# Kernel tuning notes

Hardware: AMD Instinct MI355X
Metric: run time of the kernel (lower is better)

## Reference

```python
import jax, jax.numpy as jnp
import numpy as np

B, N = 4, 512
C_IN, RES, SR = 256, 7, 2
FC_DIM = 1024
NUM_CLASSES, BOX_DIM, BINS = 3, 6, 12
OUT_CH = NUM_CLASSES * (1 + BOX_DIM + 2 * BINS) + 1  # 94
IMG = 512
STRIDES = (8, 16, 32)


def setup_inputs() -> dict:
    key = jax.random.key(0)
    ks = jax.random.split(key, 12)
    feat_p3 = jax.random.normal(ks[0], (B, C_IN, IMG // 8, IMG // 8), jnp.float32)
    feat_p4 = jax.random.normal(ks[1], (B, C_IN, IMG // 16, IMG // 16), jnp.float32)
    feat_p5 = jax.random.normal(ks[2], (B, C_IN, IMG // 32, IMG // 32), jnp.float32)
    cy = jax.random.uniform(ks[3], (B, N), minval=64.0, maxval=448.0)
    cx = jax.random.uniform(ks[4], (B, N), minval=64.0, maxval=448.0)
    h = jax.random.uniform(ks[5], (B, N), minval=16.0, maxval=120.0)
    w = jax.random.uniform(ks[6], (B, N), minval=16.0, maxval=120.0)
    bbox2d = jnp.stack([cy - h / 2, cx - w / 2, cy + h / 2, cx + w / 2], -1)  # tlbr
    anchors = jnp.stack([cy, cx, h, w], -1)  # (y, x, l, w)
    anchor_id = jax.random.randint(ks[7], (B, N), 0, 9, dtype=jnp.int32)
    flat = C_IN * RES * RES
    fc1_w = jax.random.normal(ks[8], (FC_DIM, flat), jnp.float32) * 0.01
    fc1_b = jnp.zeros((FC_DIM,), jnp.float32)
    bn1_g = jnp.ones((FC_DIM,), jnp.float32)
    bn1_b = jnp.zeros((FC_DIM,), jnp.float32)
    fc2_w = jax.random.normal(ks[9], (FC_DIM, FC_DIM), jnp.float32) * 0.02
    fc2_b = jnp.zeros((FC_DIM,), jnp.float32)
    bn2_g = jnp.ones((FC_DIM,), jnp.float32)
    bn2_b = jnp.zeros((FC_DIM,), jnp.float32)
    pred_w = jax.random.normal(ks[10], (OUT_CH, FC_DIM), jnp.float32) * 0.02
    pred_b = jnp.zeros((OUT_CH,), jnp.float32)
    return dict(feat_p3=feat_p3, feat_p4=feat_p4, feat_p5=feat_p5, bbox2d=bbox2d,
                anchors=anchors, anchor_id=anchor_id, fc1_w=fc1_w, fc1_b=fc1_b,
                bn1_g=bn1_g, bn1_b=bn1_b, fc2_w=fc2_w, fc2_b=fc2_b,
                bn2_g=bn2_g, bn2_b=bn2_b, pred_w=pred_w, pred_b=pred_b)


def _roi_align(feat, boxes, scale):
    # feat: [C,H,W]; boxes: [N,4] tlbr in image coords; aligned=True ROIAlign.
    C, H, W = feat.shape
    S = RES * SR
    t = boxes[:, 0] * scale - 0.5
    l = boxes[:, 1] * scale - 0.5
    bh = (boxes[:, 2] - boxes[:, 0]) * scale / RES  # bin height
    bw = (boxes[:, 3] - boxes[:, 1]) * scale / RES
    g = (jnp.arange(S, dtype=feat.dtype) + 0.5) / SR  # sample offsets in bin units
    ys = t[:, None] + g[None, :] * bh[:, None]  # [N,S]
    xs = l[:, None] + g[None, :] * bw[:, None]
    yc = jnp.clip(ys, 0.0, H - 1.0)
    xc = jnp.clip(xs, 0.0, W - 1.0)
    y0 = jnp.floor(yc)
    x0 = jnp.floor(xc)
    y0i = y0.astype(jnp.int32)
    x0i = x0.astype(jnp.int32)
    y1i = jnp.minimum(y0i + 1, H - 1)
    x1i = jnp.minimum(x0i + 1, W - 1)
    ly = yc - y0
    lx = xc - x0

    def gat(yi, xi):  # -> [C,N,S,S]
        return feat[:, yi[:, :, None], xi[:, None, :]]

    w00 = ((1 - ly)[:, :, None] * (1 - lx)[:, None, :])[None]
    w01 = ((1 - ly)[:, :, None] * lx[:, None, :])[None]
    w10 = (ly[:, :, None] * (1 - lx)[:, None, :])[None]
    w11 = (ly[:, :, None] * lx[:, None, :])[None]
    v = gat(y0i, x0i) * w00 + gat(y0i, x1i) * w01 + gat(y1i, x0i) * w10 + gat(y1i, x1i) * w11
    v = jnp.transpose(v, (1, 0, 2, 3)).reshape(-1, C, RES, SR, RES, SR)
    return v.mean((3, 5))  # [N,C,RES,RES] avg over sampling grid


def _bn_train(x, g, b):
    m = x.mean(0)
    v = x.var(0)
    return (x - m) * jax.lax.rsqrt(v + 1e-5) * g + b


def _forward(feat_p3, feat_p4, feat_p5, bbox2d, anchors, fc1_w, fc1_b, bn1_g, bn1_b,
             fc2_w, fc2_b, bn2_g, bn2_b, pred_w, pred_b, anchor_id):
    feats = (feat_p3, feat_p4, feat_p5)
    lvl = anchor_id // 3  # [B,N] feature-level assignment
    # box_pooler: pool every box at every level, then select its assigned level
    # (equivalent to the torch gather/sort/cat dispatch, in original box order).
    sel = 0.0
    for i, s in enumerate(STRIDES):
        pooled = jax.vmap(lambda f, bx, sc=1.0 / s: _roi_align(f, bx, sc))(feats[i], bbox2d)
        sel = sel + pooled * (lvl == i)[..., None, None, None].astype(pooled.dtype)
    x = sel.reshape(B * N, -1)  # [B*N, C*7*7]
    x = jax.nn.relu(_bn_train(x @ fc1_w.T + fc1_b, bn1_g, bn1_b))
    x = jax.nn.relu(_bn_train(x @ fc2_w.T + fc2_b, bn2_g, bn2_b))
    pred = (x @ pred_w.T + pred_b).reshape(B, N, OUT_CH)
    # decode: slice per-loss channels then apply box deltas per category
    c0 = NUM_CLASSES + 1
    cat = pred[..., :c0]  # [B,N,4]
    b1 = c0 + NUM_CLASSES * BOX_DIM
    bbox3d = pred[..., c0:b1].reshape(B, N, NUM_CLASSES, BOX_DIM)
    yaw_cls = pred[..., b1:b1 + NUM_CLASSES * BINS]
    yaw_res = pred[..., b1 + NUM_CLASSES * BINS:]
    delta = bbox3d[..., :4]  # yxlw deltas per category
    zh = bbox3d[..., 4:]
    stride_px = jnp.exp2(lvl.astype(pred.dtype) + 3.0)  # 8/16/32
    yx = anchors[:, :, None, :2] + delta[..., :2] * stride_px[..., None, None]
    lw = anchors[:, :, None, 2:] * jnp.exp(jnp.clip(delta[..., 2:], -4.0, 4.0))
    box_out = jnp.concatenate([yx, lw, zh], -1).reshape(B, N, NUM_CLASSES * BOX_DIM)
    return jnp.concatenate([cat, box_out, yaw_cls, yaw_res], -1)  # [B,N,94]


def reference(feat_p3, feat_p4, feat_p5, bbox2d, anchors, anchor_id, fc1_w, fc1_b,
              bn1_g, bn1_b, fc2_w, fc2_b, bn2_g, bn2_b, pred_w, pred_b):
    return _forward(feat_p3, feat_p4, feat_p5, bbox2d, anchors, fc1_w, fc1_b, bn1_g,
                    bn1_b, fc2_w, fc2_b, bn2_g, bn2_b, pred_w, pred_b, anchor_id)
```

## Files before the change

### kernel.cpp

```cpp
#include <hip/hip_runtime.h>
#include <hip/hip_bf16.h>

typedef __attribute__((ext_vector_type(8))) short short8;
typedef __attribute__((ext_vector_type(4))) float floatx4;
typedef __attribute__((ext_vector_type(4))) unsigned short ushort4v;

#define DEVI __device__ __forceinline__


DEVI unsigned short f2bf(float v) {
  union { __hip_bfloat16 h; unsigned short u; } cv;
  cv.h = __float2bfloat16(v);
  return cv.u;
}
DEVI short f2bfs(float v) { return (short)f2bf(v); }

DEVI void gload16(const void* gptr, void* lptr) {
  __builtin_amdgcn_global_load_lds(
      (const __attribute__((address_space(1))) unsigned int*)gptr,
      (__attribute__((address_space(3))) unsigned int*)(unsigned long long)(uintptr_t)lptr,
      16, 0, 0);
}

#define ROI_BLKS   16384
#define CVT1_END   28928
#define CVT2_END   29952
#define GRID_TOTAL 30336

__global__ __launch_bounds__(256) void prep_roi_kernel(
    const float* __restrict__ p3, const float* __restrict__ p4,
    const float* __restrict__ p5, const float* __restrict__ bbox,
    const int* __restrict__ aid, unsigned short* __restrict__ X,
    const float* __restrict__ fc1_w, unsigned short* __restrict__ W1b,
    const float* __restrict__ fc2_w, unsigned short* __restrict__ W2b,
    const float* __restrict__ pred_w, unsigned short* __restrict__ W3b) {
  constexpr int PS = 260;
  constexpr int PBS = 280;
  constexpr int PS8 = 260;
  constexpr int PBS8 = 72;
  __shared__ float Pf[32 * PS];
  __shared__ float wyx[238];
  __shared__ int sy0[14], sx0[14];
  __shared__ float sly[14], slx[14];

  const int bid = blockIdx.x;
  const int tid = threadIdx.x;

  if (bid >= ROI_BLKS) {
    if (bid < CVT1_END) {
      size_t i = (size_t)(bid - ROI_BLKS) * 256 + tid;
      float4 v = ((const float4*)fc1_w)[i];
      ushort4v o;
      o[0] = f2bf(v.x); o[1] = f2bf(v.y); o[2] = f2bf(v.z); o[3] = f2bf(v.w);
      ((ushort4v*)W1b)[i] = o;
    } else if (bid < CVT2_END) {
      size_t i = (size_t)(bid - CVT1_END) * 256 + tid;
      float4 v = ((const float4*)fc2_w)[i];
      ushort4v o;
      o[0] = f2bf(v.x); o[1] = f2bf(v.y); o[2] = f2bf(v.z); o[3] = f2bf(v.w);
      ((ushort4v*)W2b)[i] = o;
    } else {
      int i = (bid - CVT2_END) * 256 + tid;
      int row = i >> 10;
      W3b[i] = (row < 94) ? f2bf(pred_w[i]) : (unsigned short)0;
    }
    return;
  }

  unsigned short* Pb = (unsigned short*)Pf;
  const int box = bid & 2047;
  const int oct = bid >> 11;
  const int b = box >> 9;
  const int lane = tid & 63, wid = tid >> 6;

  const int lvl = aid[box] / 3;
  const int H = 64 >> lvl;
  const int HH = H * H;
  const float* base = (lvl == 0) ? p3 : ((lvl == 1) ? p4 : p5);
  const float scale = 0.125f / (float)(1 << lvl);

  if (tid < 28) {
    int s = tid;
    bool isY = s < 14;
    int k = isY ? s : s - 14;
    float lo = bbox[box * 4 + (isY ? 0 : 1)];
    float hi = bbox[box * 4 + (isY ? 2 : 3)];
    float t = lo * scale - 0.5f;
    float cell = (hi - lo) * scale * (1.0f / 7.0f);
    float pos = t + ((float)k + 0.5f) * 0.5f * cell;
    pos = fminf(fmaxf(pos, 0.0f), (float)(H - 1));
    int i0 = (int)floorf(pos);
    if (i0 > H - 2) i0 = H - 2;
    float fr = pos - (float)i0;
    if (isY) { sy0[k] = i0; sly[k] = fr; }
    else     { sx0[k] = i0; slx[k] = fr; }
  }
  __syncthreads();

  const int ry8 = min(sy0[0], H - 8), rx8 = min(sx0[0], H - 8);
  const bool fast = (sy0[13] - ry8 <= 6) && (sx0[13] - rx8 <= 6);
  const int ryb = fast ? ry8 : min(sy0[0], H - 16);
  const int rxb = fast ? rx8 : min(sx0[0], H - 16);
  const float* fb = base + ((size_t)b * 256 + oct * 32) * HH + ryb * H + rxb;

  if (tid < 224) {
    int j = tid;
    bool isY = j < 112;
    int k2 = isY ? j : j - 112;
    int py = k2 >> 4, r = k2 & 15;
    int o0 = isY ? ryb : rxb;
    float acc = 0.f;
#pragma unroll
    for (int ss = 0; ss < 2; ++ss) {
      int s = 2 * py + ss;
      int rel = (isY ? sy0[s] : sx0[s]) - o0;
      float fr = isY ? sly[s] : slx[s];
      if (r == rel)     acc += 1.0f - fr;
      if (r == rel + 1) acc += fr;
    }
    wyx[(isY ? 0 : 119) + py * 17 + r] = acc * 0.5f;
  }

  const int fr = lane & 15, fg = lane >> 4;
  const int cell = wid * 16 + fr;
  const int py = (cell * 37) >> 8;
  const int px = cell - py * 7;

  floatx4 acc0 = (floatx4){0.f, 0.f, 0.f, 0.f};
  floatx4 acc1 = (floatx4){0.f, 0.f, 0.f, 0.f};

  if (fast) {
    {
      const int r8 = (lane & 15) >> 1, c8 = (lane & 1) * 4, lch = lane >> 4;
      const float* s8 = fb + r8 * H + c8;
#pragma unroll
      for (int it = 0; it < 2; ++it) {
        int grp = it * 4 + wid;
        gload16(s8 + (size_t)(grp * 4 + lch) * HH, &Pf[grp * PS8] + lane * 4);
      }
    }
    __syncthreads();

    {
      const int cch = tid & 31, hf = tid >> 5;
      const float* src = &Pf[(cch >> 2) * PS8 + (cch & 3) * 64 + hf * 8];
      floatx4 v0 = *(const floatx4*)src, v1 = *(const floatx4*)(src + 4);
      __syncthreads();
      unsigned int d0 = (unsigned int)f2bf(v0[0]) | ((unsigned int)f2bf(v0[1]) << 16);
      unsigned int d1 = (unsigned int)f2bf(v0[2]) | ((unsigned int)f2bf(v0[3]) << 16);
      unsigned int d2 = (unsigned int)f2bf(v1[0]) | ((unsigned int)f2bf(v1[1]) << 16);
      unsigned int d3 = (unsigned int)f2bf(v1[2]) | ((unsigned int)f2bf(v1[3]) << 16);
      *(uint4*)&Pb[cch * PBS8 + hf * 8] = make_uint4(d0, d1, d2, d3);
    }

    float xv[8];
    const float* xp = &wyx[119 + px * 17];
#pragma unroll
    for (int e = 0; e < 8; ++e) xv[e] = xp[e];
    const float w0 = wyx[py * 17 + fg];
    const float w1 = wyx[py * 17 + 4 + fg];
    __syncthreads();

#pragma unroll
    for (int kk = 0; kk < 2; ++kk) {
      short8 af0 = *(const short8*)&Pb[fr * PBS8 + kk * 32 + fg * 8];
      short8 af1 = *(const short8*)&Pb[(16 + fr) * PBS8 + kk * 32 + fg * 8];
      short8 bfr;
      const float w = kk ? w1 : w0;
#pragma unroll
      for (int e = 0; e < 8; ++e) bfr[e] = f2bfs(w * xv[e]);
      acc0 = __builtin_amdgcn_mfma_f32_16x16x32_bf16(af0, bfr, acc0, 0, 0, 0);
      acc1 = __builtin_amdgcn_mfma_f32_16x16x32_bf16(af1, bfr, acc1, 0, 0, 0);
    }
  } else {
    {
      const int r = lane >> 2, c4 = (lane & 3) * 4;
      const float* src0 = fb + r * H + c4;
#pragma unroll
      for (int it = 0; it < 8; ++it) {
        int ch = it * 4 + wid;
        gload16(src0 + (size_t)ch * HH, &Pf[ch * PS] + lane * 4);
      }
    }
    __syncthreads();

    {
      const int cch = tid & 31, rp = tid >> 5;
      const float* src = &Pf[cch * PS + rp * 32];
      floatx4 v[8];
#pragma unroll
      for (int m = 0; m < 8; ++m) v[m] = *(const floatx4*)(src + 4 * m);
      __syncthreads();
      unsigned int d[16];
#pragma unroll
      for (int m = 0; m < 8; ++m) {
        d[2 * m]     = (unsigned int)f2bf(v[m][0]) | ((unsigned int)f2bf(v[m][1]) << 16);
        d[2 * m + 1] = (unsigned int)f2bf(v[m][2]) | ((unsigned int)f2bf(v[m][3]) << 16);
      }
      unsigned short* dst = &Pb[cch * PBS + rp * 32];
#pragma unroll
      for (int m = 0; m < 4; ++m)
        *(uint4*)(dst + m * 8) = make_uint4(d[4 * m], d[4 * m + 1], d[4 * m + 2], d[4 * m + 3]);
    }

    float xv[8], wyv[8];
    {
      const float* xp = &wyx[119 + px * 17 + (fg & 1) * 8];
#pragma unroll
      for (int e = 0; e < 8; ++e) xv[e] = xp[e];
      const float* wp = &wyx[py * 17 + (fg >> 1)];
#pragma unroll
      for (int kk = 0; kk < 8; ++kk) wyv[kk] = wp[2 * kk];
    }
    __syncthreads();

#pragma unroll
    for (int kk = 0; kk < 8; ++kk) {
      short8 af0 = *(const short8*)&Pb[fr * PBS + kk * 32 + fg * 8];
      short8 af1 = *(const short8*)&Pb[(16 + fr) * PBS + kk * 32 + fg * 8];
      short8 bfr;
      const float w = wyv[kk];
#pragma unroll
      for (int e = 0; e < 8; ++e) bfr[e] = f2bfs(w * xv[e]);
      acc0 = __builtin_amdgcn_mfma_f32_16x16x32_bf16(af0, bfr, acc0, 0, 0, 0);
      acc1 = __builtin_amdgcn_mfma_f32_16x16x32_bf16(af1, bfr, acc1, 0, 0, 0);
    }
  }

  if (cell < 49) {
    unsigned short* xb = X + (size_t)box * 12544 + (size_t)(oct * 32) * 49 + cell;
#pragma unroll
    for (int q = 0; q < 4; ++q) {
      xb[(fg * 4 + q) * 49] = f2bf(acc0[q]);
      xb[(16 + fg * 4 + q) * 49] = f2bf(acc1[q]);
    }
  }
}

template <int KSPLIT>
__global__ __launch_bounds__(256) void gemm_bt_swz(
    const unsigned short* __restrict__ A, const unsigned short* __restrict__ Bw,
    float* __restrict__ C, int M, int N, int K) {
  constexpr int BM = 128, BN = 128, BK = 64;
  __shared__ unsigned short As[BM * BK];
  __shared__ unsigned short Bs[BN * BK];

  const int tid = threadIdx.x;
  const int lane = tid & 63, wid = tid >> 6;
  const int wr = wid >> 1, wc = wid & 1;
  const int fr = lane & 15, fg = lane >> 4;

  int bx = blockIdx.x, by = blockIdx.y, bz = blockIdx.z;
  {
    const int gx = gridDim.x, gy = gridDim.y;
    const int nwg = gx * gy * gridDim.z;
    if ((nwg & 7) == 0) {
      int lin = bx + gx * (by + gy * bz);
      int swz = (lin & 7) * (nwg >> 3) + (lin >> 3);
      bx = swz % gx;
      int t = swz / gx;
      by = t % gy;
      bz = t / gy;
    }
  }
  const int tm = bx * BM, tn = by * BN;

  const int kLen = K / KSPLIT;
  const int kTiles = kLen / BK;
  const int kBeg = bz * kLen;
  float* Cz = C + (size_t)bz * M * N;

  floatx4 acc[4][4];
#pragma unroll
  for (int i = 0; i < 4; ++i)
#pragma unroll
    for (int j = 0; j < 4; ++j)
      acc[i][j] = (floatx4){0.f, 0.f, 0.f, 0.f};

  for (int t = 0; t < kTiles; ++t) {
    const int k0 = kBeg + t * BK;
#pragma unroll
    for (int s = tid; s < BM * 8; s += 256) {
      int row = s >> 3, sl = s & 7;
      int slg = sl ^ (row & 7);
      gload16(&A[(size_t)(tm + row) * K + k0 + slg * 8], &As[s * 8]);
    }
#pragma unroll
    for (int s = tid; s < BN * 8; s += 256) {
      int row = s >> 3, sl = s & 7;
      int slg = sl ^ (row & 7);
      gload16(&Bw[(size_t)(tn + row) * K + k0 + slg * 8], &Bs[s * 8]);
    }
    __syncthreads();

#pragma unroll
    for (int kk = 0; kk < 2; ++kk) {
      short8 af[4], bf[4];
#pragma unroll
      for (int i = 0; i < 4; ++i) {
        int row = wr * 64 + i * 16 + fr;
        int sl = (kk * 4 + fg) ^ (row & 7);
        af[i] = *reinterpret_cast<const short8*>(&As[(row * 8 + sl) * 8]);
      }
#pragma unroll
      for (int j = 0; j < 4; ++j) {
        int row = wc * 64 + j * 16 + fr;
        int sl = (kk * 4 + fg) ^ (row & 7);
        bf[j] = *reinterpret_cast<const short8*>(&Bs[(row * 8 + sl) * 8]);
      }
#pragma unroll
      for (int i = 0; i < 4; ++i)
#pragma unroll
        for (int j = 0; j < 4; ++j)
          acc[i][j] = __builtin_amdgcn_mfma_f32_16x16x32_bf16(af[i], bf[j], acc[i][j], 0, 0, 0);
    }
    __syncthreads();
  }

#pragma unroll
  for (int i = 0; i < 4; ++i)
#pragma unroll
    for (int j = 0; j < 4; ++j)
#pragma unroll
      for (int q = 0; q < 4; ++q) {
        int rr = tm + wr * 64 + i * 16 + fg * 4 + q;
        int cc = tn + wc * 64 + j * 16 + fr;
        Cz[(size_t)rr * N + cc] = acc[i][j][q];
      }
}

template <int BM, int BN, int WAVES_M, int WAVES_N, int KSPLIT>
__global__ __launch_bounds__(256) void gemm_bt_kernel(
    const unsigned short* __restrict__ A, const unsigned short* __restrict__ Bw,
    float* __restrict__ C, int M, int N, int K) {
  constexpr int BK = 32;
  constexpr int WM = BM / WAVES_M, WN = BN / WAVES_N;
  constexpr int AF = WM / 16, BF = WN / 16;
  constexpr int ASLOT = BM * 4;
  constexpr int BSLOT = BN * 4;
  __shared__ unsigned short As[BM * BK];
  __shared__ unsigned short Bs[BN * BK];

  const int tid = threadIdx.x;
  const int lane = tid & 63, wid = tid >> 6;
  const int wr = wid / WAVES_N, wc = wid % WAVES_N;
  const int tm = blockIdx.x * BM, tn = blockIdx.y * BN;
  const int fr = lane & 15, fg = lane >> 4;

  const int kLen = K / KSPLIT;
  const int kBeg = blockIdx.z * kLen;
  float* Cz = C + (size_t)blockIdx.z * M * N;

  floatx4 acc[AF][BF];
#pragma unroll
  for (int i = 0; i < AF; ++i)
#pragma unroll
    for (int j = 0; j < BF; ++j)
      acc[i][j] = (floatx4){0.f, 0.f, 0.f, 0.f};

  for (int k0 = kBeg; k0 < kBeg + kLen; k0 += BK) {
#pragma unroll
    for (int s = tid; s < ASLOT; s += 256) {
      int row = s >> 2, kb = (s & 3) << 3;
      gload16(&A[(size_t)(tm + row) * K + k0 + kb], &As[s * 8]);
    }
#pragma unroll
    for (int s = tid; s < BSLOT; s += 256) {
      int row = s >> 2, kb = (s & 3) << 3;
      gload16(&Bw[(size_t)(tn + row) * K + k0 + kb], &Bs[s * 8]);
    }
    __syncthreads();

    short8 af[AF], bfv[BF];
#pragma unroll
    for (int i = 0; i < AF; ++i)
      af[i] = *reinterpret_cast<const short8*>(&As[(wr * WM + i * 16 + fr) * BK + fg * 8]);
#pragma unroll
    for (int j = 0; j < BF; ++j)
      bfv[j] = *reinterpret_cast<const short8*>(&Bs[(wc * WN + j * 16 + fr) * BK + fg * 8]);
#pragma unroll
    for (int i = 0; i < AF; ++i)
#pragma unroll
      for (int j = 0; j < BF; ++j)
        acc[i][j] = __builtin_amdgcn_mfma_f32_16x16x32_bf16(af[i], bfv[j], acc[i][j], 0, 0, 0);
    __syncthreads();
  }

#pragma unroll
  for (int i = 0; i < AF; ++i)
#pragma unroll
    for (int j = 0; j < BF; ++j)
#pragma unroll
      for (int q = 0; q < 4; ++q) {
        int rr = tm + wr * WM + i * 16 + fg * 4 + q;
        int cc = tn + wc * WN + j * 16 + fr;
        Cz[(size_t)rr * N + cc] = acc[i][j][q];
      }
}

__global__ void bn_stats_red_kernel(const float* __restrict__ Yp, float* __restrict__ Yred,
                                    float* __restrict__ psum, float* __restrict__ psq,
                                    int Ncols, int rowsPer, int P, size_t pstride) {
  int c = blockIdx.x * blockDim.x + threadIdx.x;
  int r0 = blockIdx.y * rowsPer;
  float s = 0.f, ss = 0.f;
  for (int r = 0; r < rowsPer; ++r) {
    size_t idx = (size_t)(r0 + r) * Ncols + c;
    float v = Yp[idx];
    for (int p = 1; p < P; ++p) v += Yp[idx + (size_t)p * pstride];
    Yred[idx] = v;
    s += v;
    ss += v * v;
  }
  psum[(size_t)blockIdx.y * Ncols + c] = s;
  psq[(size_t)blockIdx.y * Ncols + c] = ss;
}

__global__ void bn_finalize_kernel(const float* __restrict__ psum, const float* __restrict__ psq,
                                   const float* __restrict__ g, const float* __restrict__ b,
                                   float* __restrict__ scale, float* __restrict__ shift,
                                   int Ncols, int P, float invM) {
  int c = blockIdx.x * blockDim.x + threadIdx.x;
  if (c >= Ncols) return;
  float s = 0.f, ss = 0.f;
  for (int p = 0; p < P; ++p) {
    s += psum[(size_t)p * Ncols + c];
    ss += psq[(size_t)p * Ncols + c];
  }
  float mean = s * invM;
  float var = ss * invM - mean * mean;
  float rstd = rsqrtf(var + 1e-5f);
  float sc = rstd * g[c];
  scale[c] = sc;
  shift[c] = b[c] - mean * sc;
}

__global__ void bn_apply4_kernel(const float4* __restrict__ Y, const float* __restrict__ scale,
                                 const float* __restrict__ shift, ushort4v* __restrict__ X,
                                 int colGroupsMask, int total4) {
  int i = blockIdx.x * blockDim.x + threadIdx.x;
  if (i >= total4) return;
  int c0 = (i & colGroupsMask) * 4;
  float4 v = Y[i];
  ushort4v o;
  o[0] = f2bf(fmaxf(v.x * scale[c0 + 0] + shift[c0 + 0], 0.0f));
  o[1] = f2bf(fmaxf(v.y * scale[c0 + 1] + shift[c0 + 1], 0.0f));
  o[2] = f2bf(fmaxf(v.z * scale[c0 + 2] + shift[c0 + 2], 0.0f));
  o[3] = f2bf(fmaxf(v.w * scale[c0 + 3] + shift[c0 + 3], 0.0f));
  X[i] = o;
}

__global__ void decode_kernel(const float* __restrict__ Y3, const float* __restrict__ pb,
                              const float* __restrict__ anchors, const int* __restrict__ aid,
                              float* __restrict__ out) {
  int i = blockIdx.x * blockDim.x + threadIdx.x;
  if (i >= 2048 * 94) return;
  int bn = i / 94;
  int ch = i - bn * 94;
  size_t idx = (size_t)bn * 96 + ch;
  float v = Y3[idx] + Y3[idx + 2048 * 96] + Y3[idx + 2 * 2048 * 96] + Y3[idx + 3 * 2048 * 96];
  v += pb[ch];
  float o = v;
  if (ch >= 4 && ch < 22) {
    int q = ch - 4;
    int d = q % 6;
    if (d < 2) {
      float stride_px = (float)(8 << (aid[bn] / 3));
      o = anchors[(size_t)bn * 4 + d] + v * stride_px;
    } else if (d < 4) {
      float cl = fminf(fmaxf(v, -4.0f), 4.0f);
      o = anchors[(size_t)bn * 4 + d] * expf(cl);
    }
  }
  out[i] = o;
}

extern "C" void kernel_launch(void* const* d_in, const int* in_sizes, int n_in,
                              void* d_out, int out_size, void* d_ws, size_t ws_size,
                              hipStream_t stream) {
  const float* feat_p3   = (const float*)d_in[0];
  const float* feat_p4   = (const float*)d_in[1];
  const float* feat_p5   = (const float*)d_in[2];
  const float* bbox2d    = (const float*)d_in[3];
  const float* anchors   = (const float*)d_in[4];
  const int*   anchor_id = (const int*)d_in[5];
  const float* fc1_w     = (const float*)d_in[6];
  const float* bn1_g     = (const float*)d_in[8];
  const float* bn1_b     = (const float*)d_in[9];
  const float* fc2_w     = (const float*)d_in[10];
  const float* bn2_g     = (const float*)d_in[12];
  const float* bn2_b     = (const float*)d_in[13];
  const float* pred_w    = (const float*)d_in[14];
  const float* pred_b    = (const float*)d_in[15];
  float* out = (float*)d_out;

  const int M = 2048;
  const int K1 = 12544;
  const int FC = 1024;
  const int RG = 128;

  char* ws = (char*)d_ws;
  auto alloc = [&](size_t bytes) -> char* {
    char* p = ws;
    ws += (bytes + 255) & ~(size_t)255;
    return p;
  };
  unsigned short* W1b  = (unsigned short*)alloc((size_t)FC * K1 * 2);
  unsigned short* W2b  = (unsigned short*)alloc((size_t)FC * FC * 2);
  unsigned short* W3b  = (unsigned short*)alloc((size_t)96 * FC * 2);
  unsigned short* X1   = (unsigned short*)alloc((size_t)M * K1 * 2);
  float*          Yp   = (float*)alloc((size_t)4 * M * FC * 4);
  float*          Yr   = (float*)alloc((size_t)M * FC * 4);
  unsigned short* X2   = (unsigned short*)alloc((size_t)M * FC * 2);
  unsigned short* X3   = (unsigned short*)alloc((size_t)M * FC * 2);
  float*          Y3   = (float*)alloc((size_t)4 * M * 96 * 4);
  float*          ps   = (float*)alloc((size_t)RG * FC * 4);
  float*          pq   = (float*)alloc((size_t)RG * FC * 4);
  float*          sc1  = (float*)alloc((size_t)FC * 4);
  float*          sh1  = (float*)alloc((size_t)FC * 4);
  float*          sc2  = (float*)alloc((size_t)FC * 4);
  float*          sh2  = (float*)alloc((size_t)FC * 4);

  prep_roi_kernel<<<GRID_TOTAL, 256, 0, stream>>>(
      feat_p3, feat_p4, feat_p5, bbox2d, anchor_id, X1,
      fc1_w, W1b, fc2_w, W2b, pred_w, W3b);

  gemm_bt_swz<4><<<dim3(M / 128, FC / 128, 4), 256, 0, stream>>>(X1, W1b, Yp, M, FC, K1);

  bn_stats_red_kernel<<<dim3(FC / 256, RG), 256, 0, stream>>>(Yp, Yr, ps, pq, FC, M / RG, 4, (size_t)M * FC);
  bn_finalize_kernel<<<FC / 256, 256, 0, stream>>>(ps, pq, bn1_g, bn1_b, sc1, sh1, FC, RG, 1.0f / M);
  bn_apply4_kernel<<<(M * FC / 4) / 256, 256, 0, stream>>>(
      (const float4*)Yr, sc1, sh1, (ushort4v*)X2, FC / 4 - 1, M * FC / 4);

  gemm_bt_swz<2><<<dim3(M / 128, FC / 128, 2), 256, 0, stream>>>(X2, W2b, Yp, M, FC, FC);

  bn_stats_red_kernel<<<dim3(FC / 256, RG), 256, 0, stream>>>(Yp, Yr, ps, pq, FC, M / RG, 2, (size_t)M * FC);
  bn_finalize_kernel<<<FC / 256, 256, 0, stream>>>(ps, pq, bn2_g, bn2_b, sc2, sh2, FC, RG, 1.0f / M);
  bn_apply4_kernel<<<(M * FC / 4) / 256, 256, 0, stream>>>(
      (const float4*)Yr, sc2, sh2, (ushort4v*)X3, FC / 4 - 1, M * FC / 4);

  gemm_bt_kernel<64, 96, 2, 2, 4><<<dim3(M / 64, 1, 4), 256, 0, stream>>>(X3, W3b, Y3, M, 96, FC);

  decode_kernel<<<(2048 * 94 + 255) / 256, 256, 0, stream>>>(Y3, pred_b, anchors, anchor_id, out);
}
```

Measured before the change: 243.6 us.

## Fuse BN stats/finalize/apply into cooperative kernel and raise split-K factors

Replaces the three batch-norm kernels per layer with one cooperative kernel that reduces split-K partials into an LDS tile, writes partial stats, grid-syncs, computes scale/shift and applies ReLU+bf16 conversion from LDS. This removes the intermediate reduced fp32 buffer round trip and two launches per layer. Split-K is also raised (7 for fc1, 4 for fc2) for better CU occupancy, at the cost of more partial-sum memory traffic and reliance on co-residency for the grid sync.

```diff
diff --git a/kernel.cpp b/kernel.cpp
--- a/kernel.cpp
+++ b/kernel.cpp
@@ -1,5 +1,8 @@
 #include <hip/hip_runtime.h>
 #include <hip/hip_bf16.h>
+#include <hip/hip_cooperative_groups.h>
+
+namespace cg = cooperative_groups;
 
 typedef __attribute__((ext_vector_type(8))) short short8;
 typedef __attribute__((ext_vector_type(4))) float floatx4;
@@ -398,56 +401,65 @@
       }
 }
 
-__global__ void bn_stats_red_kernel(const float* __restrict__ Yp, float* __restrict__ Yred,
-                                    float* __restrict__ psum, float* __restrict__ psq,
-                                    int Ncols, int rowsPer, int P, size_t pstride) {
-  int c = blockIdx.x * blockDim.x + threadIdx.x;
-  int r0 = blockIdx.y * rowsPer;
-  float s = 0.f, ss = 0.f;
-  for (int r = 0; r < rowsPer; ++r) {
-    size_t idx = (size_t)(r0 + r) * Ncols + c;
-    float v = Yp[idx];
-    for (int p = 1; p < P; ++p) v += Yp[idx + (size_t)p * pstride];
-    Yred[idx] = v;
-    s += v;
-    ss += v * v;
-  }
-  psum[(size_t)blockIdx.y * Ncols + c] = s;
-  psq[(size_t)blockIdx.y * Ncols + c] = ss;
-}
-
-__global__ void bn_finalize_kernel(const float* __restrict__ psum, const float* __restrict__ psq,
-                                   const float* __restrict__ g, const float* __restrict__ b,
-                                   float* __restrict__ scale, float* __restrict__ shift,
-                                   int Ncols, int P, float invM) {
-  int c = blockIdx.x * blockDim.x + threadIdx.x;
-  if (c >= Ncols) return;
-  float s = 0.f, ss = 0.f;
-  for (int p = 0; p < P; ++p) {
-    s += psum[(size_t)p * Ncols + c];
-    ss += psq[(size_t)p * Ncols + c];
-  }
-  float mean = s * invM;
-  float var = ss * invM - mean * mean;
-  float rstd = rsqrtf(var + 1e-5f);
-  float sc = rstd * g[c];
-  scale[c] = sc;
-  shift[c] = b[c] - mean * sc;
-}
-
-__global__ void bn_apply4_kernel(const float4* __restrict__ Y, const float* __restrict__ scale,
-                                 const float* __restrict__ shift, ushort4v* __restrict__ X,
-                                 int colGroupsMask, int total4) {
-  int i = blockIdx.x * blockDim.x + threadIdx.x;
-  if (i >= total4) return;
-  int c0 = (i & colGroupsMask) * 4;
-  float4 v = Y[i];
-  ushort4v o;
-  o[0] = f2bf(fmaxf(v.x * scale[c0 + 0] + shift[c0 + 0], 0.0f));
-  o[1] = f2bf(fmaxf(v.y * scale[c0 + 1] + shift[c0 + 1], 0.0f));
-  o[2] = f2bf(fmaxf(v.z * scale[c0 + 2] + shift[c0 + 2], 0.0f));
-  o[3] = f2bf(fmaxf(v.w * scale[c0 + 3] + shift[c0 + 3], 0.0f));
-  X[i] = o;
+__global__ __launch_bounds__(256) void bn_fused_kernel(
+    const float* __restrict__ Yp, const float* __restrict__ g,
+    const float* __restrict__ bta, unsigned short* __restrict__ X,
+    int P, size_t pstride, float* __restrict__ ps, float* __restrict__ pq,
+    float invM) {
+  constexpr int FC = 1024, TS = 264;
+  __shared__ float tile[16 * TS];
+  __shared__ float sc[256], sh[256];
+
+  const int blk = blockIdx.x;
+  const int tid = threadIdx.x;
+  const int rg = blk >> 2, cgi = blk & 3;
+  const int c = cgi * 256 + tid;
+
+  {
+    float s = 0.f, ss = 0.f;
+    for (int r = 0; r < 16; ++r) {
+      size_t idx = (size_t)(rg * 16 + r) * FC + c;
+      float v = Yp[idx];
+      for (int p = 1; p < P; ++p) v += Yp[idx + (size_t)p * pstride];
+      tile[r * TS + tid] = v;
+      s += v;
+      ss += v * v;
+    }
+    ps[(size_t)rg * FC + c] = s;
+    pq[(size_t)rg * FC + c] = ss;
+  }
+  cg::this_grid().sync();
+
+  {
+    float s = 0.f, ss = 0.f;
+    for (int p = 0; p < 128; ++p) {
+      s += ps[(size_t)p * FC + c];
+      ss += pq[(size_t)p * FC + c];
+    }
+    float mean = s * invM;
+    float var = ss * invM - mean * mean;
+    float rstd = rsqrtf(var + 1e-5f);
+    float scv = rstd * g[c];
+    sc[tid] = scv;
+    sh[tid] = bta[c] - mean * scv;
+  }
+  __syncthreads();
+
+  {
+    const int lr = tid >> 4, lc0 = (tid & 15) * 16;
+    unsigned short* xo = X + (size_t)(rg * 16 + lr) * FC + cgi * 256 + lc0;
+#pragma unroll
+    for (int m = 0; m < 4; ++m) {
+      int lc = lc0 + m * 4;
+      float4 v = *(const float4*)&tile[lr * TS + lc];
+      ushort4v o;
+      o[0] = f2bf(fmaxf(v.x * sc[lc + 0] + sh[lc + 0], 0.0f));
+      o[1] = f2bf(fmaxf(v.y * sc[lc + 1] + sh[lc + 1], 0.0f));
+      o[2] = f2bf(fmaxf(v.z * sc[lc + 2] + sh[lc + 2], 0.0f));
+      o[3] = f2bf(fmaxf(v.w * sc[lc + 3] + sh[lc + 3], 0.0f));
+      *(ushort4v*)(xo + m * 4) = o;
+    }
+  }
 }
 
 __global__ void decode_kernel(const float* __restrict__ Y3, const float* __restrict__ pb,
@@ -509,35 +521,40 @@
   unsigned short* W2b  = (unsigned short*)alloc((size_t)FC * FC * 2);
   unsigned short* W3b  = (unsigned short*)alloc((size_t)96 * FC * 2);
   unsigned short* X1   = (unsigned short*)alloc((size_t)M * K1 * 2);
-  float*          Yp   = (float*)alloc((size_t)4 * M * FC * 4);
-  float*          Yr   = (float*)alloc((size_t)M * FC * 4);
+  float*          Yp   = (float*)alloc((size_t)7 * M * FC * 4);
   unsigned short* X2   = (unsigned short*)alloc((size_t)M * FC * 2);
   unsigned short* X3   = (unsigned short*)alloc((size_t)M * FC * 2);
   float*          Y3   = (float*)alloc((size_t)4 * M * 96 * 4);
   float*          ps   = (float*)alloc((size_t)RG * FC * 4);
   float*          pq   = (float*)alloc((size_t)RG * FC * 4);
-  float*          sc1  = (float*)alloc((size_t)FC * 4);
-  float*          sh1  = (float*)alloc((size_t)FC * 4);
-  float*          sc2  = (float*)alloc((size_t)FC * 4);
-  float*          sh2  = (float*)alloc((size_t)FC * 4);
 
   prep_roi_kernel<<<GRID_TOTAL, 256, 0, stream>>>(
       feat_p3, feat_p4, feat_p5, bbox2d, anchor_id, X1,
       fc1_w, W1b, fc2_w, W2b, pred_w, W3b);
 
-  gemm_bt_swz<4><<<dim3(M / 128, FC / 128, 4), 256, 0, stream>>>(X1, W1b, Yp, M, FC, K1);
-
-  bn_stats_red_kernel<<<dim3(FC / 256, RG), 256, 0, stream>>>(Yp, Yr, ps, pq, FC, M / RG, 4, (size_t)M * FC);
-  bn_finalize_kernel<<<FC / 256, 256, 0, stream>>>(ps, pq, bn1_g, bn1_b, sc1, sh1, FC, RG, 1.0f / M);
-  bn_apply4_kernel<<<(M * FC / 4) / 256, 256, 0, stream>>>(
-      (const float4*)Yr, sc1, sh1, (ushort4v*)X2, FC / 4 - 1, M * FC / 4);
-
-  gemm_bt_swz<2><<<dim3(M / 128, FC / 128, 2), 256, 0, stream>>>(X2, W2b, Yp, M, FC, FC);
-
-  bn_stats_red_kernel<<<dim3(FC / 256, RG), 256, 0, stream>>>(Yp, Yr, ps, pq, FC, M / RG, 2, (size_t)M * FC);
-  bn_finalize_kernel<<<FC / 256, 256, 0, stream>>>(ps, pq, bn2_g, bn2_b, sc2, sh2, FC, RG, 1.0f / M);
-  bn_apply4_kernel<<<(M * FC / 4) / 256, 256, 0, stream>>>(
-      (const float4*)Yr, sc2, sh2, (ushort4v*)X3, FC / 4 - 1, M * FC / 4);
+  gemm_bt_swz<7><<<dim3(M / 128, FC / 128, 7), 256, 0, stream>>>(X1, W1b, Yp, M, FC, K1);
+
+  {
+    int P = 7;
+    size_t pstride = (size_t)M * FC;
+    float invM = 1.0f / M;
+    const float* YpC = Yp;
+    void* args[] = {(void*)&YpC, (void*)&bn1_g, (void*)&bn1_b, (void*)&X2,
+                    (void*)&P, (void*)&pstride, (void*)&ps, (void*)&pq, (void*)&invM};
+    hipLaunchCooperativeKernel((void*)bn_fused_kernel, dim3(512), dim3(256), args, 0, stream);
+  }
+
+  gemm_bt_swz<4><<<dim3(M / 128, FC / 128, 4), 256, 0, stream>>>(X2, W2b, Yp, M, FC, FC);
+
+  {
+    int P = 4;
+    size_t pstride = (size_t)M * FC;
+    float invM = 1.0f / M;
+    const float* YpC = Yp;
+    void* args[] = {(void*)&YpC, (void*)&bn2_g, (void*)&bn2_b, (void*)&X3,
+                    (void*)&P, (void*)&pstride, (void*)&ps, (void*)&pq, (void*)&invM};
+    hipLaunchCooperativeKernel((void*)bn_fused_kernel, dim3(512), dim3(256), args, 0, stream);
+  }
 
   gemm_bt_kernel<64, 96, 2, 2, 4><<<dim3(M / 64, 1, 4), 256, 0, stream>>>(X3, W3b, Y3, M, 96, FC);
 
```

Measured after the change: 376.7 us. +54.6%, slower.
